# Kernel optimization log

Hardware: AMD Instinct MI355X
Metric: run time of the kernel (lower is better)

Reference implementation:

```python
import jax, jax.numpy as jnp
import numpy as np

B, L, D = 2, 2048, 1024
H, DH = 16, 64            # heads, dim_head; inner_dim = H*DH = 1024
SCALE = DH ** -0.5


def setup_inputs() -> dict:
    key = jax.random.key(0)
    ks = jax.random.split(key, 7)
    s = 0.02
    return {
        "x": jax.random.normal(ks[0], (B, L, D), dtype=jnp.float32),
        "attention_mask": jnp.zeros((B * H, L, L), dtype=jnp.float32),
        "Wq": jax.random.normal(ks[1], (H * DH, D), dtype=jnp.float32) * s,
        "Wk": jax.random.normal(ks[2], (H * DH, D), dtype=jnp.float32) * s,
        "Wv": jax.random.normal(ks[3], (H * DH, D), dtype=jnp.float32) * s,
        "Wo": jax.random.normal(ks[4], (D, H * DH), dtype=jnp.float32) * s,
        "bo": jnp.zeros((D,), dtype=jnp.float32),
    }


def _split_heads(t):
    # [B, L, H*DH] -> [(B*H), L, DH]
    b, l, _ = t.shape
    return t.reshape(b, l, H, DH).transpose(0, 2, 1, 3).reshape(b * H, l, DH)


def reference(x, attention_mask, Wq, Wk, Wv, Wo, bo):
    # Self-attention: encoder_hidden_states = hidden_states
    q = _split_heads(jnp.einsum('bld,ed->ble', x, Wq))  # [(B*H), L, DH]
    k = _split_heads(jnp.einsum('bld,ed->ble', x, Wk))
    v = _split_heads(jnp.einsum('bld,ed->ble', x, Wv))
    # baddbmm: mask + scale * q @ k^T  -> [(B*H), L, L]
    scores = attention_mask + SCALE * jnp.einsum('nqd,nkd->nqk', q, k)
    probs = jax.nn.softmax(scores, axis=-1)
    hidden = jnp.einsum('nqk,nkd->nqd', probs, v)       # [(B*H), L, DH]
    hidden = hidden.reshape(B, H, L, DH).transpose(0, 2, 1, 3).reshape(B, L, H * DH)
    return jnp.einsum('ble,de->bld', hidden, Wo) + bo   # out projection (dropout=0)
```

## Files before the change

### kernel.cpp

```cpp
#include <hip/hip_runtime.h>


typedef __attribute__((ext_vector_type(8))) short short8;
typedef __attribute__((ext_vector_type(8))) __bf16 bf16x8;
typedef __attribute__((ext_vector_type(4))) float f32x4;

#define GLDS16(gp, lp)                                                         \
  __builtin_amdgcn_global_load_lds(                                            \
      (const __attribute__((address_space(1))) void*)(gp),                     \
      (__attribute__((address_space(3))) void*)(lp), 16, 0, 0)
#define GLDS4(gp, lp)                                                          \
  __builtin_amdgcn_global_load_lds(                                            \
      (const __attribute__((address_space(1))) void*)(gp),                     \
      (__attribute__((address_space(3))) void*)(lp), 4, 0, 0)

__device__ __forceinline__ unsigned short f2bf(float f) {
  unsigned u = __builtin_bit_cast(unsigned, f);
  u += 0x7fffu + ((u >> 16) & 1u);
  return (unsigned short)(u >> 16);
}

__global__ __launch_bounds__(256) void convert_all(
    const float* __restrict__ x, const float* __restrict__ wq,
    const float* __restrict__ wk, const float* __restrict__ wv,
    const float* __restrict__ wo, unsigned short* __restrict__ xb,
    unsigned short* __restrict__ wqkv, unsigned short* __restrict__ wob) {
  const int X4 = (2 * 2048 * 1024) / 4;
  const int W4 = (1024 * 1024) / 4;
  const int total = X4 + 4 * W4;
  for (int i = blockIdx.x * 256 + threadIdx.x; i < total;
       i += gridDim.x * 256) {
    const float* src; unsigned short* dst; int off;
    if (i < X4)               { src = x;  dst = xb;                   off = i; }
    else if (i < X4 + W4)     { src = wq; dst = wqkv;                 off = i - X4; }
    else if (i < X4 + 2 * W4) { src = wk; dst = wqkv + 1024 * 1024;   off = i - X4 - W4; }
    else if (i < X4 + 3 * W4) { src = wv; dst = wqkv + 2 * 1024 * 1024; off = i - X4 - 2 * W4; }
    else                      { src = wo; dst = wob;                  off = i - X4 - 3 * W4; }
    float4 v = ((const float4*)src)[off];
    uint2 o;
    o.x = (unsigned)f2bf(v.x) | ((unsigned)f2bf(v.y) << 16);
    o.y = (unsigned)f2bf(v.z) | ((unsigned)f2bf(v.w) << 16);
    ((uint2*)dst)[off] = o;
  }
}

template <int MODE>
__global__ __launch_bounds__(256, 2) void gemm_bt(
    const unsigned short* __restrict__ A, const unsigned short* __restrict__ Bw,
    unsigned short* __restrict__ o_q, unsigned short* __restrict__ o_k,
    unsigned short* __restrict__ o_vT, const float* __restrict__ bias,
    float* __restrict__ o_f) {
  constexpr int K = 1024;
  __shared__ unsigned short As[128 * 32];
  __shared__ unsigned short Bs[128 * 32];
  const int t = threadIdx.x;
  const int w = t >> 6;
  const int lane = t & 63;
  const int g = lane >> 4;
  const int q16 = lane & 15;
  const int wm = w >> 1, wn = w & 1;
  const int bn0 = blockIdx.x * 128, bm0 = blockIdx.y * 128;
  const int arow = t >> 2;
  const int acol = (t & 3) * 8;

  f32x4 acc[4][4];
  const f32x4 z4 = {0.f, 0.f, 0.f, 0.f};
#pragma unroll
  for (int i = 0; i < 4; ++i)
#pragma unroll
    for (int j = 0; j < 4; ++j) acc[i][j] = z4;

  for (int k0 = 0; k0 < K; k0 += 32) {
#pragma unroll
    for (int c = 0; c < 2; ++c) {
      GLDS16(A + (size_t)(bm0 + c * 64 + arow) * K + k0 + acol,
             As + c * 2048 + w * 512);
      GLDS16(Bw + (size_t)(bn0 + c * 64 + arow) * K + k0 + acol,
             Bs + c * 2048 + w * 512);
    }
    __syncthreads();
    bf16x8 af[4], bf[4];
#pragma unroll
    for (int i = 0; i < 4; ++i)
      af[i] = *(const bf16x8*)(As + (wm * 64 + i * 16 + q16) * 32 + g * 8);
#pragma unroll
    for (int j = 0; j < 4; ++j)
      bf[j] = *(const bf16x8*)(Bs + (wn * 64 + j * 16 + q16) * 32 + g * 8);
#pragma unroll
    for (int i = 0; i < 4; ++i)
#pragma unroll
      for (int j = 0; j < 4; ++j)
        acc[i][j] =
            __builtin_amdgcn_mfma_f32_16x16x32_bf16(af[i], bf[j], acc[i][j], 0, 0, 0);
    __syncthreads();
  }

  if constexpr (MODE == 0) {
    const int which = bn0 >> 10;
#pragma unroll
    for (int i = 0; i < 4; ++i)
#pragma unroll
      for (int j = 0; j < 4; ++j)
#pragma unroll
        for (int r = 0; r < 4; ++r) {
          const int m = bm0 + wm * 64 + i * 16 + g * 4 + r;
          const int n = (bn0 & 1023) + wn * 64 + j * 16 + q16;
          const float v = acc[i][j][r];
          const int bb = m >> 11, lp = m & 2047;
          const int h = n >> 6, d = n & 63;
          const int bh = bb * 16 + h;
          if (which == 0)
            o_q[((size_t)bh * 2048 + lp) * 64 + d] = f2bf(v * 0.125f);
          else if (which == 1)
            o_k[((size_t)bh * 2048 + lp) * 64 + d] = f2bf(v);
          else
            o_vT[((size_t)bh * 64 + d) * 2048 + lp] = f2bf(v);
        }
  } else {
#pragma unroll
    for (int i = 0; i < 4; ++i)
#pragma unroll
      for (int j = 0; j < 4; ++j)
#pragma unroll
        for (int r = 0; r < 4; ++r) {
          const int m = bm0 + wm * 64 + i * 16 + g * 4 + r;
          const int n = bn0 + wn * 64 + j * 16 + q16;
          o_f[(size_t)m * 1024 + n] = acc[i][j][r] + bias[n];
        }
  }
}

__global__ __launch_bounds__(256, 3) void attn_kernel(
    const unsigned short* __restrict__ kb, const unsigned short* __restrict__ qb,
    const unsigned short* __restrict__ vT, const float* __restrict__ mask,
    unsigned short* __restrict__ hb) {
  __shared__ float Mst[2][64][64];
  __shared__ unsigned short Kst[2 * 2048];
  __shared__ unsigned short Vst[2 * 2048];
  __shared__ unsigned short Plds[4][16][40];
  const int orig = blockIdx.x;
  const int bid = (orig & 7) * 128 + (orig >> 3);
  const int bh = bid >> 5, qt = bid & 31;
  const int t = threadIdx.x, w = t >> 6, lane = t & 63;
  const int g = lane >> 4, q16 = lane & 15;
  const int qrow0 = qt * 64;
  const int qrow = qrow0 + w * 16;

  const unsigned short* qptr = qb + ((size_t)bh * 2048 + qrow + q16) * 64 + g * 8;
  bf16x8 qf0 = *(const bf16x8*)(qptr);
  bf16x8 qf1 = *(const bf16x8*)(qptr + 32);

  f32x4 O[4];
  const f32x4 z4 = {0.f, 0.f, 0.f, 0.f};
#pragma unroll
  for (int dt = 0; dt < 4; ++dt) O[dt] = z4;
  float mrun = -1e30f, lsum = 0.f;

  const int rK = w * 8 + (lane >> 3), cK = (lane & 7) ^ (rK & 7);
  const unsigned short* ksrc = kb + (size_t)bh * 2048 * 64 + (size_t)rK * 64 + cK * 8;
  const int rV = w * 16 + (lane >> 2), cV = (lane & 3) ^ ((rV >> 1) & 3);
  const unsigned short* vsrc = vT + (size_t)bh * 64 * 2048 + (size_t)rV * 2048 + cV * 8;
  const float* mA = mask + ((size_t)bh * 2048 + qrow0 + w * 16) * 2048;
  const int mo_oct = (lane >> 5) & 1;
  const int mo_k = (lane >> 2) & 7;
  const int mo_j = lane & 3;

  const int x7 = q16 & 7;
  const int kx0 = (g ^ x7) * 8;
  const int kx1 = ((g + 4) ^ x7) * 8;
  const int cg0 = (g ^ x7) * 4;
  const int cg1 = ((g + 4) ^ x7) * 4;
  const int vx = (g ^ ((q16 >> 1) & 3)) * 8;

#define STAGE_M(sidx, dstbuf)                                                  \
  do {                                                                         \
    _Pragma("unroll") for (int jr = 0; jr < 16; ++jr) {                        \
      GLDS4(mA + (size_t)jr * 2048 + (sidx)*64 +                               \
                (mo_oct * 8 + (mo_k ^ (jr & 7))) * 4 + mo_j,                   \
            &Mst[dstbuf][w * 16 + jr][0]);                                     \
    }                                                                          \
  } while (0)

  GLDS16(ksrc, Kst + 0 * 2048 + w * 512);
  GLDS16(vsrc, Vst + 0 * 2048 + w * 512);
  STAGE_M(0, 0);
  GLDS16(ksrc + (size_t)1 * 2048, Kst + 1 * 2048 + w * 512);
  GLDS16(vsrc + (size_t)1 * 32, Vst + 1 * 2048 + w * 512);

  for (int tl = 0; tl < 64; ++tl) {
    const int s = tl >> 1, u = tl & 1;
    if (tl == 0)      asm volatile("s_waitcnt vmcnt(2)" ::: "memory");
    else if (u == 0)  asm volatile("s_waitcnt vmcnt(0)" ::: "memory");
    else              asm volatile("s_waitcnt vmcnt(16)" ::: "memory");
    __builtin_amdgcn_s_barrier();
    __builtin_amdgcn_sched_barrier(0);

    {
      const int tn = (tl + 1 < 64) ? tl + 1 : 63;
      GLDS16(ksrc + (size_t)tn * 2048, Kst + ((tl + 1) & 1) * 2048 + w * 512);
      GLDS16(vsrc + (size_t)tn * 32, Vst + ((tl + 1) & 1) * 2048 + w * 512);
      if (u == 0) {
        const int sn = (s + 1 < 32) ? s + 1 : 31;
        STAGE_M(sn, (s + 1) & 1);
      }
    }

    const int sb = tl & 1;
    const unsigned short* Kb = Kst + sb * 2048;
    const unsigned short* Vb = Vst + sb * 2048;

    bf16x8 vf[4];
#pragma unroll
    for (int dt = 0; dt < 4; ++dt)
      vf[dt] = *(const bf16x8*)(Vb + (dt * 16 + q16) * 32 + vx);

    bf16x8 kf0 = *(const bf16x8*)(Kb + q16 * 64 + kx0);
    bf16x8 kf1 = *(const bf16x8*)(Kb + q16 * 64 + kx1);
    bf16x8 kf2 = *(const bf16x8*)(Kb + (16 + q16) * 64 + kx0);
    bf16x8 kf3 = *(const bf16x8*)(Kb + (16 + q16) * 64 + kx1);

    f32x4 S0 = z4, S1 = z4;
    S0 = __builtin_amdgcn_mfma_f32_16x16x32_bf16(kf0, qf0, S0, 0, 0, 0);
    S0 = __builtin_amdgcn_mfma_f32_16x16x32_bf16(kf1, qf1, S0, 0, 0, 0);
    S1 = __builtin_amdgcn_mfma_f32_16x16x32_bf16(kf2, qf0, S1, 0, 0, 0);
    S1 = __builtin_amdgcn_mfma_f32_16x16x32_bf16(kf3, qf1, S1, 0, 0, 0);

    {
      const float* Mrow = &Mst[s & 1][w * 16 + q16][u * 32];
      S0 += *(const f32x4*)(Mrow + cg0);
      S1 += *(const f32x4*)(Mrow + cg1);
    }

    float lmax = fmaxf(fmaxf(fmaxf(S0[0], S0[1]), fmaxf(S0[2], S0[3])),
                       fmaxf(fmaxf(S1[0], S1[1]), fmaxf(S1[2], S1[3])));
    if (!__all(lmax <= mrun + 8.f)) {
      float pm = fmaxf(lmax, __shfl_xor(lmax, 16));
      pm = fmaxf(pm, __shfl_xor(pm, 32));
      const float mnew = fmaxf(mrun, pm);
      const float alpha = __expf(mrun - mnew);
      lsum *= alpha;
      float ar[4];
#pragma unroll
      for (int r = 0; r < 4; ++r) ar[r] = __shfl(alpha, g * 4 + r);
#pragma unroll
      for (int dt = 0; dt < 4; ++dt)
#pragma unroll
        for (int r = 0; r < 4; ++r) O[dt][r] *= ar[r];
      mrun = mnew;
    }

    float p0[4], p1[4], rs = 0.f;
#pragma unroll
    for (int r = 0; r < 4; ++r) {
      p0[r] = __expf(S0[r] - mrun);
      p1[r] = __expf(S1[r] - mrun);
      rs += p0[r] + p1[r];
    }
    lsum += rs;

    uint2 pw0, pw1;
    pw0.x = (unsigned)f2bf(p0[0]) | ((unsigned)f2bf(p0[1]) << 16);
    pw0.y = (unsigned)f2bf(p0[2]) | ((unsigned)f2bf(p0[3]) << 16);
    pw1.x = (unsigned)f2bf(p1[0]) | ((unsigned)f2bf(p1[1]) << 16);
    pw1.y = (unsigned)f2bf(p1[2]) | ((unsigned)f2bf(p1[3]) << 16);
    *(uint2*)&Plds[w][q16][g * 4] = pw0;
    *(uint2*)&Plds[w][q16][16 + g * 4] = pw1;
    bf16x8 pf = *(const bf16x8*)&Plds[w][q16][g * 8];
#pragma unroll
    for (int dt = 0; dt < 4; ++dt)
      O[dt] = __builtin_amdgcn_mfma_f32_16x16x32_bf16(pf, vf[dt], O[dt], 0, 0, 0);
  }
#undef STAGE_M

  float rsrow = lsum + __shfl_xor(lsum, 16);
  rsrow += __shfl_xor(rsrow, 32);
  float li[4];
#pragma unroll
  for (int r = 0; r < 4; ++r) li[r] = 1.f / __shfl(rsrow, g * 4 + r);
  const int b = bh >> 4, h = bh & 15;
#pragma unroll
  for (int dt = 0; dt < 4; ++dt)
#pragma unroll
    for (int r = 0; r < 4; ++r) {
      const int qg = qrow + g * 4 + r;
      hb[((size_t)b * 2048 + qg) * 1024 + h * 64 + dt * 16 + q16] =
          f2bf(O[dt][r] * li[r]);
    }
}

extern "C" void kernel_launch(void* const* d_in, const int* in_sizes, int n_in,
                              void* d_out, int out_size, void* d_ws,
                              size_t ws_size, hipStream_t stream) {
  const float* x    = (const float*)d_in[0];
  const float* mask = (const float*)d_in[1];
  const float* wq   = (const float*)d_in[2];
  const float* wk   = (const float*)d_in[3];
  const float* wv   = (const float*)d_in[4];
  const float* wo   = (const float*)d_in[5];
  const float* bo   = (const float*)d_in[6];
  float* out = (float*)d_out;
  char* ws = (char*)d_ws;

  unsigned short* xb   = (unsigned short*)(ws);
  unsigned short* wqkv = (unsigned short*)(ws + 8u * 1024 * 1024);
  unsigned short* wob  = (unsigned short*)(ws + 14u * 1024 * 1024);
  unsigned short* qbuf = (unsigned short*)(ws + 16u * 1024 * 1024);
  unsigned short* kbuf = (unsigned short*)(ws + 24u * 1024 * 1024);
  unsigned short* vTb  = (unsigned short*)(ws + 32u * 1024 * 1024);
  unsigned short* hb   = (unsigned short*)(ws + 40u * 1024 * 1024);
  (void)in_sizes; (void)n_in; (void)out_size; (void)ws_size;

  convert_all<<<2048, 256, 0, stream>>>(x, wq, wk, wv, wo, xb, wqkv, wob);
  gemm_bt<0><<<dim3(24, 32), 256, 0, stream>>>(xb, wqkv, qbuf, kbuf, vTb,
                                               nullptr, nullptr);
  attn_kernel<<<1024, 256, 0, stream>>>(kbuf, qbuf, vTb, mask, hb);
  gemm_bt<1><<<dim3(8, 32), 256, 0, stream>>>(hb, wob, nullptr, nullptr,
                                              nullptr, bo, out);
}
```

Before: 259.9 us.

## Split attention head-dim across waves with 16-row query tiles and 16B mask loads

The attention kernel now gives each block 16 query rows instead of 64, and each of the four waves owns one 16-wide slice of the head dimension. Each wave recomputes the same QK^T scores and softmax redundantly. The grid grows from 1024 to 4096 blocks. The mask is staged with 16-byte global-to-LDS loads spread across several iterations, replacing many 4-byte loads, which cuts load instruction count. In exchange, QK^T and exp work are quadrupled across waves, and K/V tiles are reloaded four times as often per query row.

```diff
diff --git a/kernel.cpp b/kernel.cpp
--- a/kernel.cpp
+++ b/kernel.cpp
@@ -9,10 +9,6 @@
   __builtin_amdgcn_global_load_lds(                                            \
       (const __attribute__((address_space(1))) void*)(gp),                     \
       (__attribute__((address_space(3))) void*)(lp), 16, 0, 0)
-#define GLDS4(gp, lp)                                                          \
-  __builtin_amdgcn_global_load_lds(                                            \
-      (const __attribute__((address_space(1))) void*)(gp),                     \
-      (__attribute__((address_space(3))) void*)(lp), 4, 0, 0)
 
 __device__ __forceinline__ unsigned short f2bf(float f) {
   unsigned u = __builtin_bit_cast(unsigned, f);
@@ -134,36 +130,33 @@
     const unsigned short* __restrict__ kb, const unsigned short* __restrict__ qb,
     const unsigned short* __restrict__ vT, const float* __restrict__ mask,
     unsigned short* __restrict__ hb) {
-  __shared__ float Mst[2][64][64];
+  __shared__ float Mst[2][16][256];
   __shared__ unsigned short Kst[2 * 2048];
   __shared__ unsigned short Vst[2 * 2048];
   __shared__ unsigned short Plds[4][16][40];
   const int orig = blockIdx.x;
-  const int bid = (orig & 7) * 128 + (orig >> 3);
-  const int bh = bid >> 5, qt = bid & 31;
+  const int bid = (orig & 7) * 512 + (orig >> 3);
+  const int bh = bid >> 7, qt = bid & 127;
   const int t = threadIdx.x, w = t >> 6, lane = t & 63;
   const int g = lane >> 4, q16 = lane & 15;
-  const int qrow0 = qt * 64;
-  const int qrow = qrow0 + w * 16;
-
-  const unsigned short* qptr = qb + ((size_t)bh * 2048 + qrow + q16) * 64 + g * 8;
+  const int qrow0 = qt * 16;
+
+  const unsigned short* qptr = qb + ((size_t)bh * 2048 + qrow0 + q16) * 64 + g * 8;
   bf16x8 qf0 = *(const bf16x8*)(qptr);
   bf16x8 qf1 = *(const bf16x8*)(qptr + 32);
 
-  f32x4 O[4];
   const f32x4 z4 = {0.f, 0.f, 0.f, 0.f};
-#pragma unroll
-  for (int dt = 0; dt < 4; ++dt) O[dt] = z4;
+  f32x4 O = z4;
   float mrun = -1e30f, lsum = 0.f;
 
   const int rK = w * 8 + (lane >> 3), cK = (lane & 7) ^ (rK & 7);
   const unsigned short* ksrc = kb + (size_t)bh * 2048 * 64 + (size_t)rK * 64 + cK * 8;
   const int rV = w * 16 + (lane >> 2), cV = (lane & 3) ^ ((rV >> 1) & 3);
   const unsigned short* vsrc = vT + (size_t)bh * 64 * 2048 + (size_t)rV * 2048 + cV * 8;
-  const float* mA = mask + ((size_t)bh * 2048 + qrow0 + w * 16) * 2048;
-  const int mo_oct = (lane >> 5) & 1;
-  const int mo_k = (lane >> 2) & 7;
-  const int mo_j = lane & 3;
+  const float* mA = mask + ((size_t)bh * 2048 + qrow0) * 2048;
+  const int mOct = lane >> 3, mChk = lane & 7;
+  const int moffE = (mOct * 8 + (mChk ^ w)) * 4;
+  const int moffO = (mOct * 8 + (mChk ^ (4 + w))) * 4;
 
   const int x7 = q16 & 7;
   const int kx0 = (g ^ x7) * 8;
@@ -172,26 +165,25 @@
   const int cg1 = ((g + 4) ^ x7) * 4;
   const int vx = (g ^ ((q16 >> 1) & 3)) * 8;
 
-#define STAGE_M(sidx, dstbuf)                                                  \
+#define STAGE_M(uu, sn, buf)                                                   \
   do {                                                                         \
-    _Pragma("unroll") for (int jr = 0; jr < 16; ++jr) {                        \
-      GLDS4(mA + (size_t)jr * 2048 + (sidx)*64 +                               \
-                (mo_oct * 8 + (mo_k ^ (jr & 7))) * 4 + mo_j,                   \
-            &Mst[dstbuf][w * 16 + jr][0]);                                     \
-    }                                                                          \
+    const int row_ = (uu)*4 + w;                                               \
+    const int off_ = ((uu)&1) ? moffO : moffE;                                 \
+    GLDS16(mA + (size_t)row_ * 2048 + (sn)*256 + off_, &Mst[buf][row_][0]);    \
   } while (0)
 
   GLDS16(ksrc, Kst + 0 * 2048 + w * 512);
   GLDS16(vsrc, Vst + 0 * 2048 + w * 512);
-  STAGE_M(0, 0);
+#pragma unroll
+  for (int u = 0; u < 4; ++u) STAGE_M(u, 0, 0);
   GLDS16(ksrc + (size_t)1 * 2048, Kst + 1 * 2048 + w * 512);
   GLDS16(vsrc + (size_t)1 * 32, Vst + 1 * 2048 + w * 512);
 
   for (int tl = 0; tl < 64; ++tl) {
-    const int s = tl >> 1, u = tl & 1;
-    if (tl == 0)      asm volatile("s_waitcnt vmcnt(2)" ::: "memory");
-    else if (u == 0)  asm volatile("s_waitcnt vmcnt(0)" ::: "memory");
-    else              asm volatile("s_waitcnt vmcnt(16)" ::: "memory");
+    const int s = tl >> 3, u = tl & 7;
+    if (tl == 0)              asm volatile("s_waitcnt vmcnt(2)" ::: "memory");
+    else if (u >= 1 && u <= 4) asm volatile("s_waitcnt vmcnt(1)" ::: "memory");
+    else                      asm volatile("s_waitcnt vmcnt(0)" ::: "memory");
     __builtin_amdgcn_s_barrier();
     __builtin_amdgcn_sched_barrier(0);
 
@@ -199,21 +191,16 @@
       const int tn = (tl + 1 < 64) ? tl + 1 : 63;
       GLDS16(ksrc + (size_t)tn * 2048, Kst + ((tl + 1) & 1) * 2048 + w * 512);
       GLDS16(vsrc + (size_t)tn * 32, Vst + ((tl + 1) & 1) * 2048 + w * 512);
-      if (u == 0) {
-        const int sn = (s + 1 < 32) ? s + 1 : 31;
-        STAGE_M(sn, (s + 1) & 1);
+      if (u < 4) {
+        const int sn = (s + 1 < 8) ? s + 1 : 7;
+        STAGE_M(u, sn, (s + 1) & 1);
       }
     }
 
-    const int sb = tl & 1;
-    const unsigned short* Kb = Kst + sb * 2048;
-    const unsigned short* Vb = Vst + sb * 2048;
-
-    bf16x8 vf[4];
-#pragma unroll
-    for (int dt = 0; dt < 4; ++dt)
-      vf[dt] = *(const bf16x8*)(Vb + (dt * 16 + q16) * 32 + vx);
-
+    const unsigned short* Kb = Kst + (tl & 1) * 2048;
+    const unsigned short* Vb = Vst + (tl & 1) * 2048;
+
+    bf16x8 vf = *(const bf16x8*)(Vb + (w * 16 + q16) * 32 + vx);
     bf16x8 kf0 = *(const bf16x8*)(Kb + q16 * 64 + kx0);
     bf16x8 kf1 = *(const bf16x8*)(Kb + q16 * 64 + kx1);
     bf16x8 kf2 = *(const bf16x8*)(Kb + (16 + q16) * 64 + kx0);
@@ -226,7 +213,7 @@
     S1 = __builtin_amdgcn_mfma_f32_16x16x32_bf16(kf3, qf1, S1, 0, 0, 0);
 
     {
-      const float* Mrow = &Mst[s & 1][w * 16 + q16][u * 32];
+      const float* Mrow = &Mst[s & 1][q16][u * 32];
       S0 += *(const f32x4*)(Mrow + cg0);
       S1 += *(const f32x4*)(Mrow + cg1);
     }
@@ -243,9 +230,7 @@
 #pragma unroll
       for (int r = 0; r < 4; ++r) ar[r] = __shfl(alpha, g * 4 + r);
 #pragma unroll
-      for (int dt = 0; dt < 4; ++dt)
-#pragma unroll
-        for (int r = 0; r < 4; ++r) O[dt][r] *= ar[r];
+      for (int r = 0; r < 4; ++r) O[r] *= ar[r];
       mrun = mnew;
     }
 
@@ -266,9 +251,7 @@
     *(uint2*)&Plds[w][q16][g * 4] = pw0;
     *(uint2*)&Plds[w][q16][16 + g * 4] = pw1;
     bf16x8 pf = *(const bf16x8*)&Plds[w][q16][g * 8];
-#pragma unroll
-    for (int dt = 0; dt < 4; ++dt)
-      O[dt] = __builtin_amdgcn_mfma_f32_16x16x32_bf16(pf, vf[dt], O[dt], 0, 0, 0);
+    O = __builtin_amdgcn_mfma_f32_16x16x32_bf16(pf, vf, O, 0, 0, 0);
   }
 #undef STAGE_M
 
@@ -279,13 +262,11 @@
   for (int r = 0; r < 4; ++r) li[r] = 1.f / __shfl(rsrow, g * 4 + r);
   const int b = bh >> 4, h = bh & 15;
 #pragma unroll
-  for (int dt = 0; dt < 4; ++dt)
-#pragma unroll
-    for (int r = 0; r < 4; ++r) {
-      const int qg = qrow + g * 4 + r;
-      hb[((size_t)b * 2048 + qg) * 1024 + h * 64 + dt * 16 + q16] =
-          f2bf(O[dt][r] * li[r]);
-    }
+  for (int r = 0; r < 4; ++r) {
+    const int qg = qrow0 + g * 4 + r;
+    hb[((size_t)b * 2048 + qg) * 1024 + h * 64 + w * 16 + q16] =
+        f2bf(O[r] * li[r]);
+  }
 }
 
 extern "C" void kernel_launch(void* const* d_in, const int* in_sizes, int n_in,
@@ -313,7 +294,7 @@
   convert_all<<<2048, 256, 0, stream>>>(x, wq, wk, wv, wo, xb, wqkv, wob);
   gemm_bt<0><<<dim3(24, 32), 256, 0, stream>>>(xb, wqkv, qbuf, kbuf, vTb,
                                                nullptr, nullptr);
-  attn_kernel<<<1024, 256, 0, stream>>>(kbuf, qbuf, vTb, mask, hb);
+  attn_kernel<<<4096, 256, 0, stream>>>(kbuf, qbuf, vTb, mask, hb);
   gemm_bt<1><<<dim3(8, 32), 256, 0, stream>>>(hb, wob, nullptr, nullptr,
                                               nullptr, bo, out);
 }
```

After: 544.4 us. +109.5%, slower.
